# Kernel tuning notes

Measured on AMD Instinct MI355X. Metric: run time of the kernel, lower is better.

Reference implementation:

```python
import jax, jax.numpy as jnp
import numpy as np

B, S, D = 4, 2048, 1024
H = 16
HD = D // H  # 64


def setup_inputs() -> dict:
    key = jax.random.key(0)
    ks = jax.random.split(key, 9)
    sc = 1.0 / np.sqrt(D)
    return {
        "hidden_states": jax.random.normal(ks[0], (B, S, D), jnp.float32),
        "Wq": jax.random.normal(ks[1], (D, D), jnp.float32) * sc,
        "bq": jnp.zeros((D,), jnp.float32),
        "Wk": jax.random.normal(ks[2], (D, D), jnp.float32) * sc,
        "bk": jnp.zeros((D,), jnp.float32),
        "Wv": jax.random.normal(ks[3], (D, D), jnp.float32) * sc,
        "bv": jnp.zeros((D,), jnp.float32),
        "Wo": jax.random.normal(ks[4], (D, D), jnp.float32) * sc,
        "bo": jnp.zeros((D,), jnp.float32),
    }


def _rope_emb(seq_len, head_dim, dtype):
    # Faithful to torch buffer: emb = cat(sin(pos*inv_freq), cos(pos*inv_freq))
    inv_freq = 1.0 / (10000.0 ** (jnp.arange(0, head_dim, 2, dtype=jnp.float32) / head_dim))
    sinusoid = jnp.arange(seq_len, dtype=jnp.float32)[:, None] * inv_freq[None, :]  # [S, hd/2]
    return jnp.concatenate([jnp.sin(sinusoid), jnp.cos(sinusoid)], axis=-1).astype(dtype)  # [S, hd]


def _rotate(x, c, s):
    # x: [B,H,S,hd]; c,s: [1,1,S,hd/2]
    x1, x2 = x[..., : HD // 2], x[..., HD // 2 :]
    return jnp.concatenate([x1 * c - x2 * s, x2 * c + x1 * s], axis=-1)


def reference(hidden_states, Wq, bq, Wk, bk, Wv, bv, Wo, bo):
    b, s, d = hidden_states.shape

    def proj(W, bias):
        y = jnp.einsum("bsd,ed->bse", hidden_states, W) + bias
        return y.reshape(b, s, H, HD).transpose(0, 2, 1, 3)  # [B,H,S,hd]

    q, k, v = proj(Wq, bq), proj(Wk, bk), proj(Wv, bv)

    emb = _rope_emb(s, HD, hidden_states.dtype)
    # NOTE: original code names first half 'cos' though the buffer stores sin first.
    c = emb[None, None, :, : HD // 2]
    sn = emb[None, None, :, HD // 2 :]
    q = _rotate(q, c, sn)
    k = _rotate(k, c, sn)

    scores = jnp.einsum("bhqd,bhkd->bhqk", q, k) / jnp.sqrt(jnp.asarray(HD, hidden_states.dtype))
    probs = jax.nn.softmax(scores, axis=-1)
    ctx = jnp.einsum("bhqk,bhkd->bhqd", probs, v)
    ctx = ctx.transpose(0, 2, 1, 3).reshape(b, s, d)  # [B,S,D]
    return jnp.einsum("bsd,ed->bse", ctx, Wo) + bo
```

## Files before the change

### kernel.cpp

```cpp
#include <hip/hip_runtime.h>
#include <cmath>

#define B_ 4
#define S_ 2048
#define D_ 1024
#define H_ 16
#define HD_ 64

typedef __attribute__((ext_vector_type(8))) _Float16 half8;
typedef __attribute__((ext_vector_type(2))) _Float16 half2t;
typedef __attribute__((ext_vector_type(2))) __fp16 fp16x2;
typedef __attribute__((ext_vector_type(4))) float floatx4;
typedef __attribute__((ext_vector_type(16))) float floatx16;
typedef __attribute__((ext_vector_type(2))) unsigned uint2v;

union H2U { unsigned u; half2t h; fp16x2 f; };
__device__ __forceinline__ unsigned hpack2(float a, float b) {
    H2U x; x.h[0] = (_Float16)a; x.h[1] = (_Float16)b; return x.u;
}
__device__ __forceinline__ unsigned pkrtz(float a, float b) {
    H2U x; x.f = __builtin_amdgcn_cvt_pkrtz(a, b); return x.u;
}
__device__ __forceinline__ float h_lo(unsigned u) { H2U x; x.u = u; return (float)x.h[0]; }
__device__ __forceinline__ float h_hi(unsigned u) { H2U x; x.u = u; return (float)x.h[1]; }

__device__ __forceinline__ void barrier_lgkm() {
    asm volatile("s_waitcnt lgkmcnt(0)\n\ts_barrier" ::: "memory");
}

__global__ __launch_bounds__(256)
void conv_all(const float* __restrict__ x, unsigned short* __restrict__ o,
              const float* __restrict__ Wq, const float* __restrict__ Wk,
              const float* __restrict__ Wv, const float* __restrict__ Wo,
              const float* __restrict__ bq, const float* __restrict__ bk,
              const float* __restrict__ bv,
              unsigned short* __restrict__ Wqkvf, unsigned short* __restrict__ Wof,
              float* __restrict__ bqkv, float2* __restrict__ tab)
{
    const int t = threadIdx.x;
    const int bx = blockIdx.x;
    if (bx < 4096) {
        const int i = (bx * 256 + t) * 8;
        const float4 a = *(const float4*)(x + i);
        const float4 b = *(const float4*)(x + i + 4);
        *(uint4*)(o + i) = make_uint4(hpack2(a.x, a.y), hpack2(a.z, a.w),
                                      hpack2(b.x, b.y), hpack2(b.z, b.w));
        return;
    }
    const int bxx = bx - 4096;
    if (bxx < 2048) {
        const int w = bxx >> 9;
        const int i = ((bxx & 511) * 256 + t) * 8;
        const float* src = (w == 0) ? Wq : (w == 1) ? Wk : (w == 2) ? Wv : Wo;
        const float4 a = *(const float4*)(src + i);
        const float4 b = *(const float4*)(src + i + 4);
        const uint4 v = make_uint4(hpack2(a.x, a.y), hpack2(a.z, a.w),
                                   hpack2(b.x, b.y), hpack2(b.z, b.w));
        if (w < 3)
            *(uint4*)(Wqkvf + (size_t)w * 1048576 + i) = v;
        else
            *(uint4*)(Wof + i) = v;
    } else if (bxx == 2048) {
        const int idx = t * 4;
        *(float4*)(bqkv + idx)        = *(const float4*)(bq + idx);
        *(float4*)(bqkv + 1024 + idx) = *(const float4*)(bk + idx);
        *(float4*)(bqkv + 2048 + idx) = *(const float4*)(bv + idx);
    } else {
        const int idx = (bxx - 2049) * 256 + t;
        const int s = idx >> 5, d = idx & 31;
        const float kfreq = 0.28782313662425572f;
        const float fd = expf(-(float)d * kfreq);
        const float tt = (float)s * fd;
        tab[idx] = make_float2(sinf(tt), cosf(tt));
    }
}

template<int MODE>
__global__ __launch_bounds__(256, 2)
void gemm_half(const unsigned short* __restrict__ Ap, const unsigned short* __restrict__ Bp,
               const float* __restrict__ bias, void* __restrict__ C0,
               void* __restrict__ C1, void* __restrict__ C2,
               const float2* __restrict__ Tab,
               int M, int N, int K)
{
    __shared__ uint4 ASH[512];
    __shared__ uint4 BSH[512];

    const int tid = threadIdx.x;
    const int bm = blockIdx.x * 128;
    const int bn = blockIdx.y * 128;
    const int w = tid >> 6, l = tid & 63;
    const int wm = (w & 1) * 64, wn = (w >> 1) * 64;

    floatx4 acc[4][4];
#pragma unroll
    for (int i = 0; i < 4; ++i)
#pragma unroll
        for (int j = 0; j < 4; ++j)
#pragma unroll
            for (int r = 0; r < 4; ++r) acc[i][j][r] = 0.f;

    const int r0 = tid >> 1, scb = (tid & 1) * 2;
    const size_t ga = (size_t)(bm + r0) * K + scb * 8;
    const size_t gb = (size_t)(bn + r0) * K + scb * 8;
    const int blk = r0 >> 4, r15 = r0 & 15;
    const int p1 = (scb << 4) + r15;
    const int f0a = (blk << 6) + (p1 ^ (scb << 1));
    const int f0b = (blk << 6) + ((p1 + 16) ^ ((scb + 1) << 1));

    const half8* pA = (const half8*)ASH;
    const half8* pB = (const half8*)BSH;
    const int lg = l ^ ((l >> 4) << 1);
    const int am = (wm >> 4) * 64 + lg;
    const int bnf = (wn >> 4) * 64 + lg;

    uint4 vA0 = *(const uint4*)(Ap + ga);
    uint4 vA1 = *(const uint4*)(Ap + ga + 8);
    uint4 vB0 = *(const uint4*)(Bp + gb);
    uint4 vB1 = *(const uint4*)(Bp + gb + 8);

    for (int k0 = 0; k0 < K; k0 += 32) {
        __syncthreads();
        ASH[f0a] = vA0; ASH[f0b] = vA1;
        BSH[f0a] = vB0; BSH[f0b] = vB1;
        __syncthreads();

        const int kn = (k0 + 32 < K) ? k0 + 32 : k0;
        vA0 = *(const uint4*)(Ap + ga + kn);
        vA1 = *(const uint4*)(Ap + ga + kn + 8);
        vB0 = *(const uint4*)(Bp + gb + kn);
        vB1 = *(const uint4*)(Bp + gb + kn + 8);

        half8 a[4];
#pragma unroll
        for (int i = 0; i < 4; ++i) a[i] = pA[am + i * 64];
#pragma unroll
        for (int j = 0; j < 4; ++j) {
            const half8 b = pB[bnf + j * 64];
#pragma unroll
            for (int i = 0; i < 4; ++i)
                acc[i][j] = __builtin_amdgcn_mfma_f32_16x16x32_f16(a[i], b, acc[i][j], 0, 0, 0);
        }
    }

    const int cr = (l >> 4) << 2;
    const int cc = l & 15;

    if (MODE == 0) {
#pragma unroll
        for (int j = 0; j < 4; ++j) {
            const int col = bn + wn + j * 16 + cc;
            const float bv = bias[col];
#pragma unroll
            for (int i = 0; i < 4; ++i) {
                const int row = bm + wm + i * 16 + cr;
#pragma unroll
                for (int r = 0; r < 4; ++r) {
                    ((float*)C0)[(size_t)(row + r) * N + col] = acc[i][j][r] + bv;
                }
            }
        }
    } else {
        const int reg = bn >> 10;
        if (reg < 2) {
            const float KSs = (reg == 1) ? 0.18033688011112042f : 1.0f;
            unsigned short* dst0 = (unsigned short*)((reg == 0) ? C0 : C1);
            const int hbase = (bn - (reg << 10)) + wn;
#pragma unroll
            for (int j = 0; j < 2; ++j) {
                const int d = j * 16 + cc;
                const float b1 = bias[bn + wn + j * 16 + cc];
                const float b2 = bias[bn + wn + j * 16 + cc + 32];
#pragma unroll
                for (int i = 0; i < 4; ++i) {
                    const int row0 = bm + wm + i * 16 + cr;
#pragma unroll
                    for (int r = 0; r < 4; ++r) {
                        const int row = row0 + r;
                        const int s = row & (S_ - 1);
                        const float2 sc2 = Tab[s * 32 + d];
                        const float sn = sc2.x, cs = sc2.y;
                        const float x1 = acc[i][j][r] + b1;
                        const float x2 = acc[i][j + 2][r] + b2;
                        const float o1 = (x1 * sn - x2 * cs) * KSs;
                        const float o2 = (x2 * sn + x1 * cs) * KSs;
                        unsigned short* p = dst0 + (size_t)row * D_ + hbase + d;
                        p[0]  = (unsigned short)(hpack2(o1, o1) & 0xffffu);
                        p[32] = (unsigned short)(hpack2(o2, o2) & 0xffffu);
                    }
                }
            }
        } else {
#pragma unroll
            for (int j = 0; j < 4; ++j) {
                const int col = bn + wn + j * 16 + cc;
                const float bv = bias[col];
                const int vcol = col - 2048;
                const int h = vcol >> 6, dd = vcol & 63;
#pragma unroll
                for (int i = 0; i < 4; ++i) {
                    const int row0 = bm + wm + i * 16 + cr;
                    const int b = row0 >> 11, s = row0 & (S_ - 1);
                    const float v0 = acc[i][j][0] + bv;
                    const float v1 = acc[i][j][1] + bv;
                    const float v2 = acc[i][j][2] + bv;
                    const float v3 = acc[i][j][3] + bv;
                    unsigned short* p = (unsigned short*)C2 +
                        ((size_t)((b * H_ + h) * 64 + dd)) * S_ + s;
                    *(uint2*)p = make_uint2(hpack2(v0, v1), hpack2(v2, v3));
                }
            }
        }
    }
}

__global__ __launch_bounds__(256)
void attn_mfma32(const unsigned short* __restrict__ Qf,
                 const unsigned short* __restrict__ Kfi,
                 const unsigned short* __restrict__ Vt,
                 unsigned short* __restrict__ Cf)
{
    __shared__ uint4 KF[2][512];
    __shared__ uint4 VF[2][512];

    const int t = threadIdx.x;
    const int i = blockIdx.x;
    const int xcd = i & 7, j = i >> 3;
    const int bh = xcd * 8 + (j >> 4);
    const int qblk = j & 15;
    const int b = bh >> 4, h = bh & 15;

    const int w = t >> 6, l = t & 63;
    const int lq = l & 31, h5 = l >> 5;
    const int qrow = qblk * 128 + w * 32 + lq;

    half8 qf[4];
    const unsigned short* qp = Qf + ((size_t)(b * S_ + qrow)) * D_ + h * 64 + h5 * 8;
#pragma unroll
    for (int kc = 0; kc < 4; ++kc) qf[kc] = *(const half8*)(qp + kc * 16);

    floatx16 o0, o1, o2, z16;
#pragma unroll
    for (int r = 0; r < 16; ++r) { o0[r] = 0.f; o1[r] = 0.f; o2[r] = 0.f; z16[r] = 0.f; }

    union { unsigned u[4]; half8 s; } onesf;
    const unsigned ov = (lq == 0) ? 0x3C003C00u : 0u;
    onesf.u[0] = ov; onesf.u[1] = ov; onesf.u[2] = ov; onesf.u[3] = ov;

    const int sr = t >> 2, sc = t & 3;
    const unsigned short* gK0 = Kfi + ((size_t)(b * S_ + sr)) * D_ + h * 64 + sc * 16;
    const unsigned short* gV0 = Vt + ((size_t)((b * H_ + h) * 64 + sr)) * S_ + sc * 16;
    const int e0 = (sr >> 5) * 256 + sc * 64 + ((sr & 31) ^ (sc << 1));
    const int lx[4] = { l, l ^ 2, l ^ 4, l ^ 6 };

    uint4 ka  = *(const uint4*)(gK0);
    uint4 kb2 = *(const uint4*)(gK0 + 8);
    uint4 va  = *(const uint4*)(gV0);
    uint4 vb2 = *(const uint4*)(gV0 + 8);
    KF[0][e0] = ka; KF[0][e0 + 32] = kb2;
    VF[0][e0] = va; VF[0][e0 + 32] = vb2;
    {
        const unsigned short* gK = gK0 + (size_t)64 * D_;
        const unsigned short* gV = gV0 + 64;
        ka  = *(const uint4*)(gK);
        kb2 = *(const uint4*)(gK + 8);
        va  = *(const uint4*)(gV);
        vb2 = *(const uint4*)(gV + 8);
    }
    __syncthreads();

    for (int kt = 0; kt < 32; ++kt) {
        const int cur = kt & 1;

        if (kt < 31) {
            uint4* wK = KF[cur ^ 1];
            uint4* wV = VF[cur ^ 1];
            wK[e0] = ka; wK[e0 + 32] = kb2;
            wV[e0] = va; wV[e0 + 32] = vb2;
        }
        if (kt < 30) {
            const unsigned short* gK = gK0 + (size_t)(kt + 2) * 64 * D_;
            const unsigned short* gV = gV0 + (size_t)(kt + 2) * 64;
            ka  = *(const uint4*)(gK);
            kb2 = *(const uint4*)(gK + 8);
            va  = *(const uint4*)(gV);
            vb2 = *(const uint4*)(gV + 8);
        }

        const half8* pKc = (const half8*)KF[cur];
        const half8* pVc = (const half8*)VF[cur];

        __builtin_amdgcn_s_setprio(1);
        floatx16 st0 = __builtin_amdgcn_mfma_f32_32x32x16_f16(pKc[lx[0]],           qf[0], z16, 0, 0, 0);
        floatx16 st1 = __builtin_amdgcn_mfma_f32_32x32x16_f16(pKc[4 * 64 + lx[0]],  qf[0], z16, 0, 0, 0);
#pragma unroll
        for (int kc = 1; kc < 4; ++kc) {
            st0 = __builtin_amdgcn_mfma_f32_32x32x16_f16(pKc[kc * 64 + lx[kc]],       qf[kc], st0, 0, 0, 0);
            st1 = __builtin_amdgcn_mfma_f32_32x32x16_f16(pKc[(4 + kc) * 64 + lx[kc]], qf[kc], st1, 0, 0, 0);
        }
        __builtin_amdgcn_s_setprio(0);

        unsigned pu0[8], pu1[8];
#pragma unroll
        for (int g = 0; g < 8; ++g) {
            pu0[g] = pkrtz(__builtin_amdgcn_exp2f(st0[2 * g]),
                           __builtin_amdgcn_exp2f(st0[2 * g + 1]));
            pu1[g] = pkrtz(__builtin_amdgcn_exp2f(st1[2 * g]),
                           __builtin_amdgcn_exp2f(st1[2 * g + 1]));
        }

        __builtin_amdgcn_s_setprio(1);
#pragma unroll
        for (int kc = 0; kc < 4; ++kc) {
            const unsigned* pus = (kc >> 1) ? pu1 : pu0;
            const int g0 = (kc & 1) * 4;
            const uint2v r02 = __builtin_amdgcn_permlane32_swap(pus[g0 + 0], pus[g0 + 2], false, false);
            const uint2v r13 = __builtin_amdgcn_permlane32_swap(pus[g0 + 1], pus[g0 + 3], false, false);
            union { unsigned u[4]; half8 s; } pf;
            pf.u[0] = r02[0];
            pf.u[1] = r13[0];
            pf.u[2] = r02[1];
            pf.u[3] = r13[1];
            o0 = __builtin_amdgcn_mfma_f32_32x32x16_f16(pVc[kc * 64 + lx[kc]],       pf.s, o0, 0, 0, 0);
            o1 = __builtin_amdgcn_mfma_f32_32x32x16_f16(pVc[(4 + kc) * 64 + lx[kc]], pf.s, o1, 0, 0, 0);
            o2 = __builtin_amdgcn_mfma_f32_32x32x16_f16(onesf.s,                     pf.s, o2, 0, 0, 0);
        }
        __builtin_amdgcn_s_setprio(0);

        if (kt < 31) barrier_lgkm();
    }

    union { float f; unsigned u; } lc; lc.f = o2[0];
    const uint2v lr = __builtin_amdgcn_permlane32_swap(lc.u, lc.u, false, false);
    union { unsigned u; float f; } ls; ls.u = lr[0];
    const float inv = 1.0f / ls.f;

    const size_t cbase = ((size_t)(b * S_ + qrow)) * D_ + h * 64;
#pragma unroll
    for (int rq = 0; rq < 4; ++rq) {
        const int d0 = rq * 8 + h5 * 4;
        const uint2 y0 = make_uint2(hpack2(o0[4*rq+0] * inv, o0[4*rq+1] * inv),
                                    hpack2(o0[4*rq+2] * inv, o0[4*rq+3] * inv));
        const uint2 y1 = make_uint2(hpack2(o1[4*rq+0] * inv, o1[4*rq+1] * inv),
                                    hpack2(o1[4*rq+2] * inv, o1[4*rq+3] * inv));
        *(uint2*)(Cf + cbase + d0)      = y0;
        *(uint2*)(Cf + cbase + 32 + d0) = y1;
    }
}

extern "C" void kernel_launch(void* const* d_in, const int* in_sizes, int n_in,
                              void* d_out, int out_size, void* d_ws, size_t ws_size,
                              hipStream_t stream) {
    (void)in_sizes; (void)n_in; (void)out_size; (void)ws_size;
    const float* X  = (const float*)d_in[0];
    const float* Wq = (const float*)d_in[1];
    const float* bq = (const float*)d_in[2];
    const float* Wk = (const float*)d_in[3];
    const float* bk = (const float*)d_in[4];
    const float* Wv = (const float*)d_in[5];
    const float* bv = (const float*)d_in[6];
    const float* Wo = (const float*)d_in[7];
    const float* bo = (const float*)d_in[8];
    float* out = (float*)d_out;

    char* ws = (char*)d_ws;
#define OFF(mb) (ws + ((size_t)(mb) << 20))
    unsigned short* Xf    = (unsigned short*)OFF(0);
    unsigned short* Qf    = (unsigned short*)OFF(64);
    unsigned short* Kfb   = (unsigned short*)OFF(80);
    unsigned short* Vtb   = (unsigned short*)OFF(96);
    unsigned short* Wqkvf = (unsigned short*)OFF(112);
    unsigned short* Wof   = (unsigned short*)OFF(118);
    float*          bqkv  = (float*)OFF(120);
    float2*         rtab  = (float2*)OFF(121);
    unsigned short* Cf    = (unsigned short*)OFF(0);
#undef OFF

    conv_all<<<6401, 256, 0, stream>>>(X, Xf, Wq, Wk, Wv, Wo, bq, bk, bv,
                                       Wqkvf, Wof, bqkv, rtab);
    gemm_half<1><<<dim3(64, 24), 256, 0, stream>>>(Xf, Wqkvf, bqkv,
                                                   Qf, Kfb, Vtb, rtab,
                                                   B_*S_, 3 * D_, D_);
    attn_mfma32<<<1024, 256, 0, stream>>>(Qf, Kfb, Vtb, Cf);
    gemm_half<0><<<dim3(64, 8), 256, 0, stream>>>(Cf, Wof, bo, out, nullptr, nullptr,
                                                  nullptr, B_*S_, D_, D_);
}
```

Measured before the change: 295.0 us.

## Fuse input fp32-to-fp16 conversion into QKV GEMM and enlarge attention blocks

Drops the separate pass that converts the hidden states to fp16; the QKV GEMM now loads fp32 activations directly and packs them to fp16 in registers. This removes one full read and write of the activation tensor, at the cost of twice as many bytes loaded per A tile inside the GEMM. Separately, the attention kernel moves to 512-thread blocks covering 256 query rows, so each K/V tile staged in shared memory is reused by eight waves instead of four, and each thread loads half as much per tile.

```diff
diff --git a/kernel.cpp b/kernel.cpp
--- a/kernel.cpp
+++ b/kernel.cpp
@@ -29,8 +29,7 @@
 }
 
 __global__ __launch_bounds__(256)
-void conv_all(const float* __restrict__ x, unsigned short* __restrict__ o,
-              const float* __restrict__ Wq, const float* __restrict__ Wk,
+void conv_all(const float* __restrict__ Wq, const float* __restrict__ Wk,
               const float* __restrict__ Wv, const float* __restrict__ Wo,
               const float* __restrict__ bq, const float* __restrict__ bk,
               const float* __restrict__ bv,
@@ -38,16 +37,7 @@
               float* __restrict__ bqkv, float2* __restrict__ tab)
 {
     const int t = threadIdx.x;
-    const int bx = blockIdx.x;
-    if (bx < 4096) {
-        const int i = (bx * 256 + t) * 8;
-        const float4 a = *(const float4*)(x + i);
-        const float4 b = *(const float4*)(x + i + 4);
-        *(uint4*)(o + i) = make_uint4(hpack2(a.x, a.y), hpack2(a.z, a.w),
-                                      hpack2(b.x, b.y), hpack2(b.z, b.w));
-        return;
-    }
-    const int bxx = bx - 4096;
+    const int bxx = blockIdx.x;
     if (bxx < 2048) {
         const int w = bxx >> 9;
         const int i = ((bxx & 511) * 256 + t) * 8;
@@ -77,7 +67,7 @@
 
 template<int MODE>
 __global__ __launch_bounds__(256, 2)
-void gemm_half(const unsigned short* __restrict__ Ap, const unsigned short* __restrict__ Bp,
+void gemm_half(const void* __restrict__ Av, const unsigned short* __restrict__ Bp,
                const float* __restrict__ bias, void* __restrict__ C0,
                void* __restrict__ C1, void* __restrict__ C2,
                const float2* __restrict__ Tab,
@@ -114,8 +104,26 @@
     const int am = (wm >> 4) * 64 + lg;
     const int bnf = (wn >> 4) * 64 + lg;
 
-    uint4 vA0 = *(const uint4*)(Ap + ga);
-    uint4 vA1 = *(const uint4*)(Ap + ga + 8);
+    auto loadA = [&](int kn, uint4& A0, uint4& A1) {
+        if (MODE == 1) {
+            const float* Ap = (const float*)Av;
+            const float4 a0 = *(const float4*)(Ap + ga + kn);
+            const float4 a1 = *(const float4*)(Ap + ga + kn + 4);
+            const float4 a2 = *(const float4*)(Ap + ga + kn + 8);
+            const float4 a3 = *(const float4*)(Ap + ga + kn + 12);
+            A0 = make_uint4(hpack2(a0.x, a0.y), hpack2(a0.z, a0.w),
+                            hpack2(a1.x, a1.y), hpack2(a1.z, a1.w));
+            A1 = make_uint4(hpack2(a2.x, a2.y), hpack2(a2.z, a2.w),
+                            hpack2(a3.x, a3.y), hpack2(a3.z, a3.w));
+        } else {
+            const unsigned short* Ap = (const unsigned short*)Av;
+            A0 = *(const uint4*)(Ap + ga + kn);
+            A1 = *(const uint4*)(Ap + ga + kn + 8);
+        }
+    };
+
+    uint4 vA0, vA1;
+    loadA(0, vA0, vA1);
     uint4 vB0 = *(const uint4*)(Bp + gb);
     uint4 vB1 = *(const uint4*)(Bp + gb + 8);
 
@@ -126,8 +134,7 @@
         __syncthreads();
 
         const int kn = (k0 + 32 < K) ? k0 + 32 : k0;
-        vA0 = *(const uint4*)(Ap + ga + kn);
-        vA1 = *(const uint4*)(Ap + ga + kn + 8);
+        loadA(kn, vA0, vA1);
         vB0 = *(const uint4*)(Bp + gb + kn);
         vB1 = *(const uint4*)(Bp + gb + kn + 8);
 
@@ -214,7 +221,7 @@
     }
 }
 
-__global__ __launch_bounds__(256)
+__global__ __launch_bounds__(512)
 void attn_mfma32(const unsigned short* __restrict__ Qf,
                  const unsigned short* __restrict__ Kfi,
                  const unsigned short* __restrict__ Vt,
@@ -226,13 +233,13 @@
     const int t = threadIdx.x;
     const int i = blockIdx.x;
     const int xcd = i & 7, j = i >> 3;
-    const int bh = xcd * 8 + (j >> 4);
-    const int qblk = j & 15;
+    const int bh = xcd * 8 + (j >> 3);
+    const int qblk = j & 7;
     const int b = bh >> 4, h = bh & 15;
 
     const int w = t >> 6, l = t & 63;
     const int lq = l & 31, h5 = l >> 5;
-    const int qrow = qblk * 128 + w * 32 + lq;
+    const int qrow = qblk * 256 + w * 32 + lq;
 
     half8 qf[4];
     const unsigned short* qp = Qf + ((size_t)(b * S_ + qrow)) * D_ + h * 64 + h5 * 8;
@@ -247,25 +254,21 @@
     const unsigned ov = (lq == 0) ? 0x3C003C00u : 0u;
     onesf.u[0] = ov; onesf.u[1] = ov; onesf.u[2] = ov; onesf.u[3] = ov;
 
-    const int sr = t >> 2, sc = t & 3;
-    const unsigned short* gK0 = Kfi + ((size_t)(b * S_ + sr)) * D_ + h * 64 + sc * 16;
-    const unsigned short* gV0 = Vt + ((size_t)((b * H_ + h) * 64 + sr)) * S_ + sc * 16;
-    const int e0 = (sr >> 5) * 256 + sc * 64 + ((sr & 31) ^ (sc << 1));
+    const int sr = t >> 3, hc = t & 7, scq = hc >> 1;
+    const unsigned short* gK0 = Kfi + ((size_t)(b * S_ + sr)) * D_ + h * 64 + hc * 8;
+    const unsigned short* gV0 = Vt + ((size_t)((b * H_ + h) * 64 + sr)) * S_ + hc * 8;
+    const int e0 = (sr >> 5) * 256 + scq * 64 + ((sr & 31) ^ (scq << 1)) + (hc & 1) * 32;
     const int lx[4] = { l, l ^ 2, l ^ 4, l ^ 6 };
 
-    uint4 ka  = *(const uint4*)(gK0);
-    uint4 kb2 = *(const uint4*)(gK0 + 8);
-    uint4 va  = *(const uint4*)(gV0);
-    uint4 vb2 = *(const uint4*)(gV0 + 8);
-    KF[0][e0] = ka; KF[0][e0 + 32] = kb2;
-    VF[0][e0] = va; VF[0][e0 + 32] = vb2;
+    uint4 ka = *(const uint4*)(gK0);
+    uint4 va = *(const uint4*)(gV0);
+    KF[0][e0] = ka;
+    VF[0][e0] = va;
     {
         const unsigned short* gK = gK0 + (size_t)64 * D_;
         const unsigned short* gV = gV0 + 64;
-        ka  = *(const uint4*)(gK);
-        kb2 = *(const uint4*)(gK + 8);
-        va  = *(const uint4*)(gV);
-        vb2 = *(const uint4*)(gV + 8);
+        ka = *(const uint4*)(gK);
+        va = *(const uint4*)(gV);
     }
     __syncthreads();
 
@@ -273,18 +276,14 @@
         const int cur = kt & 1;
 
         if (kt < 31) {
-            uint4* wK = KF[cur ^ 1];
-            uint4* wV = VF[cur ^ 1];
-            wK[e0] = ka; wK[e0 + 32] = kb2;
-            wV[e0] = va; wV[e0 + 32] = vb2;
+            KF[cur ^ 1][e0] = ka;
+            VF[cur ^ 1][e0] = va;
         }
         if (kt < 30) {
             const unsigned short* gK = gK0 + (size_t)(kt + 2) * 64 * D_;
             const unsigned short* gV = gV0 + (size_t)(kt + 2) * 64;
-            ka  = *(const uint4*)(gK);
-            kb2 = *(const uint4*)(gK + 8);
-            va  = *(const uint4*)(gV);
-            vb2 = *(const uint4*)(gV + 8);
+            ka = *(const uint4*)(gK);
+            va = *(const uint4*)(gV);
         }
 
         const half8* pKc = (const half8*)KF[cur];
@@ -365,7 +364,6 @@
 
     char* ws = (char*)d_ws;
 #define OFF(mb) (ws + ((size_t)(mb) << 20))
-    unsigned short* Xf    = (unsigned short*)OFF(0);
     unsigned short* Qf    = (unsigned short*)OFF(64);
     unsigned short* Kfb   = (unsigned short*)OFF(80);
     unsigned short* Vtb   = (unsigned short*)OFF(96);
@@ -376,12 +374,12 @@
     unsigned short* Cf    = (unsigned short*)OFF(0);
 #undef OFF
 
-    conv_all<<<6401, 256, 0, stream>>>(X, Xf, Wq, Wk, Wv, Wo, bq, bk, bv,
+    conv_all<<<2305, 256, 0, stream>>>(Wq, Wk, Wv, Wo, bq, bk, bv,
                                        Wqkvf, Wof, bqkv, rtab);
-    gemm_half<1><<<dim3(64, 24), 256, 0, stream>>>(Xf, Wqkvf, bqkv,
+    gemm_half<1><<<dim3(64, 24), 256, 0, stream>>>(X, Wqkvf, bqkv,
                                                    Qf, Kfb, Vtb, rtab,
                                                    B_*S_, 3 * D_, D_);
-    attn_mfma32<<<1024, 256, 0, stream>>>(Qf, Kfb, Vtb, Cf);
+    attn_mfma32<<<512, 512, 0, stream>>>(Qf, Kfb, Vtb, Cf);
     gemm_half<0><<<dim3(64, 8), 256, 0, stream>>>(Cf, Wof, bo, out, nullptr, nullptr,
                                                   nullptr, B_*S_, D_, D_);
 }
```

Measured after the change: 313.5 us. 6.2% more time.
